# Optimization experiments

Hardware: AMD Instinct MI355X
Metric: run time of the kernel (lower is better)

The kernel has to match this reference:

```python
import jax, jax.numpy as jnp
import numpy as np

NUM_HEADS = 32
NUM_GROUP_HEADS = 8
DIM_MODEL = 2048
DIM_K = 64
DIM_V = 64


def setup_inputs() -> dict:
    key = jax.random.key(0)
    ks = jax.random.split(key, 11)
    B, S = 1, 2048
    scale = 0.02
    inp = {
        "queries": jax.random.normal(ks[0], (B, S, DIM_MODEL), jnp.float32),
        "keys": jax.random.normal(ks[1], (B, S, DIM_MODEL), jnp.float32),
        "values": jax.random.normal(ks[2], (B, S, DIM_MODEL), jnp.float32),
        "Wq": jax.random.normal(ks[3], (DIM_MODEL, DIM_K * NUM_HEADS), jnp.float32) * scale,
        "bq": jnp.zeros((DIM_K * NUM_HEADS,), jnp.float32),
        "Wk": jax.random.normal(ks[4], (DIM_MODEL, DIM_K * NUM_GROUP_HEADS), jnp.float32) * scale,
        "bk": jnp.zeros((DIM_K * NUM_GROUP_HEADS,), jnp.float32),
        "Wv": jax.random.normal(ks[5], (DIM_MODEL, DIM_V * NUM_GROUP_HEADS), jnp.float32) * scale,
        "bv": jnp.zeros((DIM_V * NUM_GROUP_HEADS,), jnp.float32),
        "Wo": jax.random.normal(ks[6], (DIM_V * NUM_HEADS, DIM_MODEL), jnp.float32) * scale,
        "bo": jnp.zeros((DIM_MODEL,), jnp.float32),
    }
    return inp


def reference(queries, keys, values, Wq, bq, Wk, bk, Wv, bv, Wo, bo):
    B, Sq, _ = queries.shape
    _, Sk, _ = keys.shape
    H, G = NUM_HEADS, NUM_GROUP_HEADS
    repeats = H // G

    # projections -> [B, heads, S, d]
    q = (queries @ Wq + bq).reshape(B, Sq, H, DIM_K).transpose(0, 2, 1, 3)
    k = (keys @ Wk + bk).reshape(B, Sk, G, DIM_K).transpose(0, 2, 1, 3)
    v = (values @ Wv + bv).reshape(B, Sk, G, DIM_V).transpose(0, 2, 1, 3)

    # GQA: repeat each group head `repeats` times (repeat_interleave on head dim)
    k = jnp.repeat(k, repeats, axis=1)  # [B, H, Sk, dk]
    v = jnp.repeat(v, repeats, axis=1)  # [B, H, Sk, dv]

    scores = jnp.einsum("bhqd,bhkd->bhqk", q, k) / (DIM_K ** 0.5)
    causal = jnp.triu(jnp.ones((Sq, Sk), dtype=bool), k=1)
    scores = jnp.where(causal, -jnp.inf, scores)
    attn = jax.nn.softmax(scores, axis=-1)
    out = jnp.einsum("bhqk,bhkd->bhqd", attn, v)  # [B, H, Sq, dv]
    out = out.transpose(0, 2, 1, 3).reshape(B, Sq, H * DIM_V)
    return out @ Wo + bo
```

## Files before the change

### kernel.cpp

```cpp
#include <hip/hip_runtime.h>
#include <hip/hip_bf16.h>

#define S_LEN  2048
#define DMODEL 2048
#define NH     32
#define NG     8
#define DK     64
#define DV     64

typedef short bf16x8 __attribute__((ext_vector_type(8)));
typedef float f32x4  __attribute__((ext_vector_type(4)));

__device__ __forceinline__ ushort f32_to_bf16(float f) {
    uint u = __float_as_uint(f);
    return (ushort)((u + 0x7fffu + ((u >> 16) & 1u)) >> 16);
}
__device__ __forceinline__ float bf16_to_f32(ushort h) {
    return __uint_as_float(((uint)h) << 16);
}
__device__ __forceinline__ uint pack_bf16x2(float a, float b) {
    return (uint)f32_to_bf16(a) | ((uint)f32_to_bf16(b) << 16);
}

__global__ void cast_f32_to_bf16(const float* __restrict__ in,
                                 ushort* __restrict__ out, int n8) {
    int i = blockIdx.x * blockDim.x + threadIdx.x;
    const int stride = gridDim.x * blockDim.x;
    for (; i < n8; i += stride) {
        const float4 a = ((const float4*)in)[2 * i];
        const float4 b = ((const float4*)in)[2 * i + 1];
        uint4 o;
        o.x = (uint)f32_to_bf16(a.x) | ((uint)f32_to_bf16(a.y) << 16);
        o.y = (uint)f32_to_bf16(a.z) | ((uint)f32_to_bf16(a.w) << 16);
        o.z = (uint)f32_to_bf16(b.x) | ((uint)f32_to_bf16(b.y) << 16);
        o.w = (uint)f32_to_bf16(b.z) | ((uint)f32_to_bf16(b.w) << 16);
        ((uint4*)out)[i] = o;
    }
}

__global__ void transpose_cast_bf16(const float* __restrict__ W,
                                    ushort* __restrict__ Wt, int K, int N) {
    __shared__ float t[32][33];
    const int n0 = blockIdx.x * 32, k0 = blockIdx.y * 32;
    const int tx = threadIdx.x, ty = threadIdx.y;
#pragma unroll
    for (int i = 0; i < 4; ++i)
        t[ty + 8 * i][tx] = W[(size_t)(k0 + ty + 8 * i) * N + n0 + tx];
    __syncthreads();
#pragma unroll
    for (int i = 0; i < 4; ++i)
        Wt[(size_t)(n0 + ty + 8 * i) * K + k0 + tx] = f32_to_bf16(t[tx][ty + 8 * i]);
}

__global__ void transpose_bf16(const ushort* __restrict__ in,
                               ushort* __restrict__ out, int R, int C) {
    __shared__ ushort t[32][34];
    const int c0 = blockIdx.x * 32, r0 = blockIdx.y * 32;
    const int tx = threadIdx.x, ty = threadIdx.y;
#pragma unroll
    for (int i = 0; i < 4; ++i)
        t[ty + 8 * i][tx] = in[(size_t)(r0 + ty + 8 * i) * C + c0 + tx];
    __syncthreads();
#pragma unroll
    for (int i = 0; i < 4; ++i)
        out[(size_t)(c0 + ty + 8 * i) * R + r0 + tx] = t[tx][ty + 8 * i];
}

template <bool OUT_F32>
__device__ __forceinline__ void gemm_body_128x64(
        const ushort* __restrict__ A, const ushort* __restrict__ Bt,
        const float* __restrict__ bias, void* __restrict__ Cv,
        ushort* As, ushort* Bs, int N, int K, float scale) {
    const int tid  = threadIdx.x;
    const int lane = tid & 63, wave = tid >> 6;
    const int l15 = lane & 15, quad = lane >> 4;
    const int row0 = blockIdx.y * 128, col0 = blockIdx.x * 64;

    f32x4 acc[2][4];
#pragma unroll
    for (int i = 0; i < 2; ++i)
#pragma unroll
        for (int j = 0; j < 4; ++j) { f32x4 z = {0.f,0.f,0.f,0.f}; acc[i][j] = z; }

    const int ar = tid >> 1, ak = (tid & 1) * 16;
    const int br = tid >> 2, bk = (tid & 3) * 8;
    const ushort* aptr = A  + (size_t)(row0 + ar) * K + ak;
    const ushort* bptr = Bt + (size_t)(col0 + br) * K + bk;

    bf16x8 a0 = *(const bf16x8*)(aptr);
    bf16x8 a1 = *(const bf16x8*)(aptr + 8);
    bf16x8 b0 = *(const bf16x8*)(bptr);

    for (int k0 = 0; k0 < K; k0 += 32) {
        __syncthreads();
        *(bf16x8*)&As[ar * 40 + ak]     = a0;
        *(bf16x8*)&As[ar * 40 + ak + 8] = a1;
        *(bf16x8*)&Bs[br * 40 + bk]     = b0;
        __syncthreads();

        if (k0 + 32 < K) {
            a0 = *(const bf16x8*)(aptr + k0 + 32);
            a1 = *(const bf16x8*)(aptr + k0 + 40);
            b0 = *(const bf16x8*)(bptr + k0 + 32);
        }

        bf16x8 af[2], bf[4];
#pragma unroll
        for (int mi = 0; mi < 2; ++mi)
            af[mi] = *(const bf16x8*)&As[(wave * 32 + mi * 16 + l15) * 40 + quad * 8];
#pragma unroll
        for (int ni = 0; ni < 4; ++ni)
            bf[ni] = *(const bf16x8*)&Bs[(ni * 16 + l15) * 40 + quad * 8];
#pragma unroll
        for (int mi = 0; mi < 2; ++mi)
#pragma unroll
            for (int ni = 0; ni < 4; ++ni)
                acc[mi][ni] = __builtin_amdgcn_mfma_f32_16x16x32_bf16(
                    af[mi], bf[ni], acc[mi][ni], 0, 0, 0);
    }

#pragma unroll
    for (int mi = 0; mi < 2; ++mi)
#pragma unroll
        for (int ni = 0; ni < 4; ++ni) {
            const int col = col0 + ni * 16 + l15;
            const float bv = bias[col];
#pragma unroll
            for (int reg = 0; reg < 4; ++reg) {
                const int row = row0 + wave * 32 + mi * 16 + quad * 4 + reg;
                const float val = (acc[mi][ni][reg] + bv) * scale;
                if (OUT_F32)
                    ((float*)Cv)[(size_t)row * N + col] = val;
                else
                    ((ushort*)Cv)[(size_t)row * N + col] = f32_to_bf16(val);
            }
        }
}

template <bool OUT_F32>
__global__ __launch_bounds__(256) void gemm_bf16_v2(
        const ushort* __restrict__ A, const ushort* __restrict__ Bt,
        const float* __restrict__ bias, void* __restrict__ Cv, int N, int K,
        float scale) {
    __shared__ ushort As[128 * 40];
    __shared__ ushort Bs[64 * 40];
    gemm_body_128x64<OUT_F32>(A, Bt, bias, Cv, As, Bs, N, K, scale);
}

__global__ __launch_bounds__(256) void gemm_kv(
        const ushort* __restrict__ Xk, const ushort* __restrict__ Xv,
        const ushort* __restrict__ Wkt, const ushort* __restrict__ Wvt,
        const float* __restrict__ bk, const float* __restrict__ bv,
        ushort* __restrict__ Kb, ushort* __restrict__ Vb, int N, int K) {
    __shared__ ushort As[128 * 40];
    __shared__ ushort Bs[64 * 40];
    if (blockIdx.z == 0)
        gemm_body_128x64<false>(Xk, Wkt, bk, Kb, As, Bs, N, K, 1.0f);
    else
        gemm_body_128x64<false>(Xv, Wvt, bv, Vb, As, Bs, N, K, 1.0f);
}

__global__ __launch_bounds__(256) void gqa_attn_mfma(
        const ushort* __restrict__ Qb, const ushort* __restrict__ Kb,
        const ushort* __restrict__ Vt, ushort* __restrict__ Ab) {
    __shared__ ushort Ks[64 * 72];
    __shared__ ushort Vs[64 * 72];
    __shared__ ushort Ps[4][16 * 72];

    const int h    = blockIdx.y, g = h >> 2;
    const int tid  = threadIdx.x;
    const int lane = tid & 63, wave = tid >> 6;
    const int l15  = lane & 15, quad = lane >> 4;
    const int NT   = S_LEN / 64;
    const float DEFER_THR = 11.5416f;

    const int srow = tid >> 2, sch = tid & 3;
    const ushort* kbase = Kb + (size_t)srow * (NG * DK) + g * DK + sch * 16;
    const ushort* vbase = Vt + (size_t)(g * 64 + srow) * S_LEN + sch * 16;

    for (int sel = 0; sel < 2; ++sel) {
        const int qt = sel ? (NT - 1 - (int)blockIdx.x) : (int)blockIdx.x;
        const int qr = qt * 64 + wave * 16;

        bf16x8 qa0, qa1;
        {
            const size_t base = (size_t)(qr + l15) * (NH * DK) + (size_t)h * DK + quad * 8;
            qa0 = *(const bf16x8*)&Qb[base];
            qa1 = *(const bf16x8*)&Qb[base + 32];
        }

        f32x4 o[4];
#pragma unroll
        for (int dt = 0; dt < 4; ++dt) { f32x4 z = {0.f,0.f,0.f,0.f}; o[dt] = z; }
        float m = -1e30f;
        float l = 0.f;

        bf16x8 kr0 = *(const bf16x8*)(kbase);
        bf16x8 kr1 = *(const bf16x8*)(kbase + 8);
        bf16x8 vr0 = *(const bf16x8*)(vbase);
        bf16x8 vr1 = *(const bf16x8*)(vbase + 8);

        for (int jt = 0; jt <= qt; ++jt) {
            __syncthreads();
            *(bf16x8*)&Ks[srow * 72 + sch * 16]     = kr0;
            *(bf16x8*)&Ks[srow * 72 + sch * 16 + 8] = kr1;
            *(bf16x8*)&Vs[srow * 72 + sch * 16]     = vr0;
            *(bf16x8*)&Vs[srow * 72 + sch * 16 + 8] = vr1;
            __syncthreads();

            if (jt < qt) {
                const size_t ko = (size_t)(jt + 1) * 64 * (NG * DK);
                const size_t vo = (size_t)(jt + 1) * 64;
                kr0 = *(const bf16x8*)(kbase + ko);
                kr1 = *(const bf16x8*)(kbase + ko + 8);
                vr0 = *(const bf16x8*)(vbase + vo);
                vr1 = *(const bf16x8*)(vbase + vo + 8);
            }

            f32x4 s[4];
#pragma unroll
            for (int kt = 0; kt < 4; ++kt) {
                const bf16x8 kb0 = *(const bf16x8*)&Ks[(kt * 16 + l15) * 72 + quad * 8];
                const bf16x8 kb1 = *(const bf16x8*)&Ks[(kt * 16 + l15) * 72 + 32 + quad * 8];
                f32x4 acc = {0.f, 0.f, 0.f, 0.f};
                acc = __builtin_amdgcn_mfma_f32_16x16x32_bf16(kb0, qa0, acc, 0, 0, 0);
                acc = __builtin_amdgcn_mfma_f32_16x16x32_bf16(kb1, qa1, acc, 0, 0, 0);
                s[kt] = acc;
            }

            if (jt == qt) {
                const int row = wave * 16 + l15;
#pragma unroll
                for (int kt = 0; kt < 4; ++kt)
#pragma unroll
                    for (int r = 0; r < 4; ++r) {
                        const int key = kt * 16 + quad * 4 + r;
                        if (key > row) s[kt][r] = -1e30f;
                    }
            }

            float pmax;
            {
                const float t0 = fmaxf(fmaxf(s[0][0], s[0][1]), fmaxf(s[0][2], s[0][3]));
                const float t1 = fmaxf(fmaxf(s[1][0], s[1][1]), fmaxf(s[1][2], s[1][3]));
                const float t2 = fmaxf(fmaxf(s[2][0], s[2][1]), fmaxf(s[2][2], s[2][3]));
                const float t3 = fmaxf(fmaxf(s[3][0], s[3][1]), fmaxf(s[3][2], s[3][3]));
                pmax = fmaxf(fmaxf(t0, t1), fmaxf(t2, t3));
            }
            pmax = fmaxf(pmax, __shfl_xor(pmax, 16, 64));
            pmax = fmaxf(pmax, __shfl_xor(pmax, 32, 64));

            if (!__all(pmax - m <= DEFER_THR)) {
                const float mnew  = fmaxf(m, pmax);
                const float alpha = __builtin_amdgcn_exp2f(m - mnew);
                l *= alpha;
#pragma unroll
                for (int dt = 0; dt < 4; ++dt)
#pragma unroll
                    for (int r = 0; r < 4; ++r) o[dt][r] *= alpha;
                m = mnew;
            }

            float p[4][4];
#pragma unroll
            for (int kt = 0; kt < 4; ++kt)
#pragma unroll
                for (int r = 0; r < 4; ++r)
                    p[kt][r] = __builtin_amdgcn_exp2f(s[kt][r] - m);

            float rsum;
            {
                const float u0 = (p[0][0] + p[0][1]) + (p[0][2] + p[0][3]);
                const float u1 = (p[1][0] + p[1][1]) + (p[1][2] + p[1][3]);
                const float u2 = (p[2][0] + p[2][1]) + (p[2][2] + p[2][3]);
                const float u3 = (p[3][0] + p[3][1]) + (p[3][2] + p[3][3]);
                rsum = (u0 + u1) + (u2 + u3);
            }
            rsum += __shfl_xor(rsum, 16, 64);
            rsum += __shfl_xor(rsum, 32, 64);
            l += rsum;

            ushort* Pw = &Ps[wave][0];
#pragma unroll
            for (int kt = 0; kt < 4; ++kt) {
                uint2 uu;
                uu.x = pack_bf16x2(p[kt][0], p[kt][1]);
                uu.y = pack_bf16x2(p[kt][2], p[kt][3]);
                *(uint2*)&Pw[l15 * 72 + kt * 16 + quad * 4] = uu;
            }
            const bf16x8 pa0 = *(const bf16x8*)&Pw[l15 * 72 + quad * 8];
            const bf16x8 pa1 = *(const bf16x8*)&Pw[l15 * 72 + 32 + quad * 8];

#pragma unroll
            for (int dt = 0; dt < 4; ++dt) {
                const bf16x8 vb0 = *(const bf16x8*)&Vs[(dt * 16 + l15) * 72 + quad * 8];
                const bf16x8 vb1 = *(const bf16x8*)&Vs[(dt * 16 + l15) * 72 + 32 + quad * 8];
                o[dt] = __builtin_amdgcn_mfma_f32_16x16x32_bf16(vb0, pa0, o[dt], 0, 0, 0);
                o[dt] = __builtin_amdgcn_mfma_f32_16x16x32_bf16(vb1, pa1, o[dt], 0, 0, 0);
            }
        }

        const float invl = 1.0f / l;
#pragma unroll
        for (int dt = 0; dt < 4; ++dt) {
            uint2 uu;
            uu.x = pack_bf16x2(o[dt][0] * invl, o[dt][1] * invl);
            uu.y = pack_bf16x2(o[dt][2] * invl, o[dt][3] * invl);
            *(uint2*)&Ab[(size_t)(qr + l15) * (NH * DV) + (size_t)h * DV + dt * 16 + quad * 4] = uu;
        }
    }
}

extern "C" void kernel_launch(void* const* d_in, const int* in_sizes, int n_in,
                              void* d_out, int out_size, void* d_ws, size_t ws_size,
                              hipStream_t stream) {
    const float* queries = (const float*)d_in[0];
    const float* keys    = (const float*)d_in[1];
    const float* values  = (const float*)d_in[2];
    const float* Wq      = (const float*)d_in[3];
    const float* bq      = (const float*)d_in[4];
    const float* Wk      = (const float*)d_in[5];
    const float* bk      = (const float*)d_in[6];
    const float* Wv      = (const float*)d_in[7];
    const float* bv      = (const float*)d_in[8];
    const float* Wo      = (const float*)d_in[9];
    const float* bo      = (const float*)d_in[10];
    float* out = (float*)d_out;

    const size_t MB = 1024 * 1024;
    unsigned char* w = (unsigned char*)d_ws;
    ushort* Xq  = (ushort*)(w + 0 * MB);
    ushort* Xk  = (ushort*)(w + 8 * MB);
    ushort* Xv  = (ushort*)(w + 16 * MB);
    ushort* Wqt = (ushort*)(w + 24 * MB);
    ushort* Wkt = (ushort*)(w + 32 * MB);
    ushort* Wvt = (ushort*)(w + 34 * MB);
    ushort* Wot = (ushort*)(w + 36 * MB);
    ushort* Qb  = (ushort*)(w + 44 * MB);
    ushort* Kb  = (ushort*)(w + 52 * MB);
    ushort* Vb  = (ushort*)(w + 54 * MB);
    ushort* Ab  = (ushort*)(w + 56 * MB);
    ushort* Vtp = (ushort*)(w + 8 * MB);

    const int n8 = (S_LEN * DMODEL) / 8;
    cast_f32_to_bf16<<<1024, 256, 0, stream>>>(queries, Xq, n8);
    cast_f32_to_bf16<<<1024, 256, 0, stream>>>(keys,    Xk, n8);
    cast_f32_to_bf16<<<1024, 256, 0, stream>>>(values,  Xv, n8);

    dim3 tb(32, 8);
    transpose_cast_bf16<<<dim3(2048 / 32, 2048 / 32), tb, 0, stream>>>(Wq, Wqt, DMODEL, 2048);
    transpose_cast_bf16<<<dim3(512 / 32,  2048 / 32), tb, 0, stream>>>(Wk, Wkt, DMODEL, 512);
    transpose_cast_bf16<<<dim3(512 / 32,  2048 / 32), tb, 0, stream>>>(Wv, Wvt, DMODEL, 512);
    transpose_cast_bf16<<<dim3(2048 / 32, 2048 / 32), tb, 0, stream>>>(Wo, Wot, DMODEL, 2048);

    const float QSCALE = 0.125f * 1.44269504f;
    gemm_bf16_v2<false><<<dim3(2048 / 64, 2048 / 128), 256, 0, stream>>>(
        Xq, Wqt, bq, Qb, 2048, DMODEL, QSCALE);
    gemm_kv<<<dim3(512 / 64, 2048 / 128, 2), 256, 0, stream>>>(
        Xk, Xv, Wkt, Wvt, bk, bv, Kb, Vb, 512, DMODEL);

    transpose_bf16<<<dim3(512 / 32, 2048 / 32), tb, 0, stream>>>(Vb, Vtp, S_LEN, 512);

    gqa_attn_mfma<<<dim3(16, 32), 256, 0, stream>>>(Qb, Kb, Vtp, Ab);

    gemm_bf16_v2<true><<<dim3(2048 / 64, 2048 / 128), 256, 0, stream>>>(
        Ab, Wot, bo, out, 2048, DMODEL, 1.0f);
}
```

Baseline: 303.3 us.

## Use direct global-to-LDS loads with double-buffered tiles in bf16 GEMMs

The projection GEMM body now loads A and B tiles with global_load_lds straight into shared memory instead of going through registers. It double-buffers the tiles so the next k-slice is fetched while MFMAs run on the current one, which removes one __syncthreads per iteration and the register staging. The trade-off is that the LDS layout loses its padding (row stride 32 instead of 40), so fragment reads may now hit bank conflicts. Correctness also depends on the barrier waiting for the outstanding async LDS loads.

```diff
diff --git a/kernel.cpp b/kernel.cpp
--- a/kernel.cpp
+++ b/kernel.cpp
@@ -20,6 +20,12 @@
 }
 __device__ __forceinline__ uint pack_bf16x2(float a, float b) {
     return (uint)f32_to_bf16(a) | ((uint)f32_to_bf16(b) << 16);
+}
+
+typedef __attribute__((address_space(3))) uint lds_uint;
+typedef const __attribute__((address_space(1))) uint g_uint;
+__device__ __forceinline__ void gload16(const void* g, void* l) {
+    __builtin_amdgcn_global_load_lds((g_uint*)g, (lds_uint*)l, 16, 0, 0);
 }
 
 __global__ void cast_f32_to_bf16(const float* __restrict__ in,
@@ -70,7 +76,8 @@
 __device__ __forceinline__ void gemm_body_128x64(
         const ushort* __restrict__ A, const ushort* __restrict__ Bt,
         const float* __restrict__ bias, void* __restrict__ Cv,
-        ushort* As, ushort* Bs, int N, int K, float scale) {
+        ushort* As, ushort* Bs,
+        int N, int K, float scale) {
     const int tid  = threadIdx.x;
     const int lane = tid & 63, wave = tid >> 6;
     const int l15 = lane & 15, quad = lane >> 4;
@@ -82,41 +89,45 @@
 #pragma unroll
         for (int j = 0; j < 4; ++j) { f32x4 z = {0.f,0.f,0.f,0.f}; acc[i][j] = z; }
 
-    const int ar = tid >> 1, ak = (tid & 1) * 16;
-    const int br = tid >> 2, bk = (tid & 3) * 8;
-    const ushort* aptr = A  + (size_t)(row0 + ar) * K + ak;
-    const ushort* bptr = Bt + (size_t)(col0 + br) * K + bk;
-
-    bf16x8 a0 = *(const bf16x8*)(aptr);
-    bf16x8 a1 = *(const bf16x8*)(aptr + 8);
-    bf16x8 b0 = *(const bf16x8*)(bptr);
-
+    const int sr = wave * 16 + (lane >> 2);
+    const int sc = (lane & 3) * 8;
+    const ushort* ga0 = A  + (size_t)(row0 + sr) * K + sc;
+    const ushort* ga1 = A  + (size_t)(row0 + 64 + sr) * K + sc;
+    const ushort* gb0 = Bt + (size_t)(col0 + sr) * K + sc;
+    ushort* lA0 = As + wave * 512;
+    ushort* lA1 = As + 2048 + wave * 512;
+    ushort* lB0 = Bs + wave * 512;
+
+    gload16(ga0, lA0);
+    gload16(ga1, lA1);
+    gload16(gb0, lB0);
+
+    int cur = 0;
     for (int k0 = 0; k0 < K; k0 += 32) {
         __syncthreads();
-        *(bf16x8*)&As[ar * 40 + ak]     = a0;
-        *(bf16x8*)&As[ar * 40 + ak + 8] = a1;
-        *(bf16x8*)&Bs[br * 40 + bk]     = b0;
-        __syncthreads();
-
         if (k0 + 32 < K) {
-            a0 = *(const bf16x8*)(aptr + k0 + 32);
-            a1 = *(const bf16x8*)(aptr + k0 + 40);
-            b0 = *(const bf16x8*)(bptr + k0 + 32);
-        }
+            const int nxt = cur ^ 1;
+            gload16(ga0 + k0 + 32, lA0 + nxt * 4096);
+            gload16(ga1 + k0 + 32, lA1 + nxt * 4096);
+            gload16(gb0 + k0 + 32, lB0 + nxt * 2048);
+        }
+        const ushort* Ac = As + cur * 4096;
+        const ushort* Bc = Bs + cur * 2048;
 
         bf16x8 af[2], bf[4];
 #pragma unroll
         for (int mi = 0; mi < 2; ++mi)
-            af[mi] = *(const bf16x8*)&As[(wave * 32 + mi * 16 + l15) * 40 + quad * 8];
+            af[mi] = *(const bf16x8*)&Ac[(wave * 32 + mi * 16 + l15) * 32 + quad * 8];
 #pragma unroll
         for (int ni = 0; ni < 4; ++ni)
-            bf[ni] = *(const bf16x8*)&Bs[(ni * 16 + l15) * 40 + quad * 8];
+            bf[ni] = *(const bf16x8*)&Bc[(ni * 16 + l15) * 32 + quad * 8];
 #pragma unroll
         for (int mi = 0; mi < 2; ++mi)
 #pragma unroll
             for (int ni = 0; ni < 4; ++ni)
                 acc[mi][ni] = __builtin_amdgcn_mfma_f32_16x16x32_bf16(
                     af[mi], bf[ni], acc[mi][ni], 0, 0, 0);
+        cur ^= 1;
     }
 
 #pragma unroll
@@ -142,8 +153,8 @@
         const ushort* __restrict__ A, const ushort* __restrict__ Bt,
         const float* __restrict__ bias, void* __restrict__ Cv, int N, int K,
         float scale) {
-    __shared__ ushort As[128 * 40];
-    __shared__ ushort Bs[64 * 40];
+    __shared__ ushort As[2 * 128 * 32];
+    __shared__ ushort Bs[2 * 64 * 32];
     gemm_body_128x64<OUT_F32>(A, Bt, bias, Cv, As, Bs, N, K, scale);
 }
 
@@ -152,8 +163,8 @@
         const ushort* __restrict__ Wkt, const ushort* __restrict__ Wvt,
         const float* __restrict__ bk, const float* __restrict__ bv,
         ushort* __restrict__ Kb, ushort* __restrict__ Vb, int N, int K) {
-    __shared__ ushort As[128 * 40];
-    __shared__ ushort Bs[64 * 40];
+    __shared__ ushort As[2 * 128 * 32];
+    __shared__ ushort Bs[2 * 64 * 32];
     if (blockIdx.z == 0)
         gemm_body_128x64<false>(Xk, Wkt, bk, Kb, As, Bs, N, K, 1.0f);
     else
```

Result: slower. 309.9 us (+2.2%).

## Merge cast, weight-transpose and QKV GEMM launches; fuse V transpose into epilogue

Applied to the files above, without the earlier changes.

The three input casts become one launch over a z-grid, and the four weight transpose-casts become one launch. The Q, K and V projections run as a single GEMM launch. The V projection writes its output already transposed through a shared-memory staging tile, so the separate V transpose kernel goes away. This cuts kernel launch count and one global round trip of V. The cost is idle blocks in the merged QKV grid (z=1,2 only use 8 of 32 x-blocks) and a larger shared-memory footprint.

```diff
diff --git a/kernel.cpp b/kernel.cpp
--- a/kernel.cpp
+++ b/kernel.cpp
@@ -22,8 +22,14 @@
     return (uint)f32_to_bf16(a) | ((uint)f32_to_bf16(b) << 16);
 }
 
-__global__ void cast_f32_to_bf16(const float* __restrict__ in,
-                                 ushort* __restrict__ out, int n8) {
+__global__ void cast3_f32_to_bf16(const float* __restrict__ q,
+                                  const float* __restrict__ k,
+                                  const float* __restrict__ v,
+                                  ushort* __restrict__ xq,
+                                  ushort* __restrict__ xk,
+                                  ushort* __restrict__ xv, int n8) {
+    const float* in  = blockIdx.z == 0 ? q  : (blockIdx.z == 1 ? k  : v);
+    ushort*      out = blockIdx.z == 0 ? xq : (blockIdx.z == 1 ? xk : xv);
     int i = blockIdx.x * blockDim.x + threadIdx.x;
     const int stride = gridDim.x * blockDim.x;
     for (; i < n8; i += stride) {
@@ -38,10 +44,20 @@
     }
 }
 
-__global__ void transpose_cast_bf16(const float* __restrict__ W,
-                                    ushort* __restrict__ Wt, int K, int N) {
+__global__ void transpose_cast4(const float* __restrict__ Wq,
+                                const float* __restrict__ Wk,
+                                const float* __restrict__ Wv,
+                                const float* __restrict__ Wo,
+                                ushort* __restrict__ Wqt, ushort* __restrict__ Wkt,
+                                ushort* __restrict__ Wvt, ushort* __restrict__ Wot) {
     __shared__ float t[32][33];
-    const int n0 = blockIdx.x * 32, k0 = blockIdx.y * 32;
+    int bx = blockIdx.x;
+    const float* W; ushort* Wt; int N;
+    if (bx < 64)      { W = Wq; Wt = Wqt; N = 2048; }
+    else if (bx < 80) { W = Wk; Wt = Wkt; N = 512;  bx -= 64; }
+    else if (bx < 96) { W = Wv; Wt = Wvt; N = 512;  bx -= 80; }
+    else              { W = Wo; Wt = Wot; N = 2048; bx -= 96; }
+    const int n0 = bx * 32, k0 = blockIdx.y * 32;
     const int tx = threadIdx.x, ty = threadIdx.y;
 #pragma unroll
     for (int i = 0; i < 4; ++i)
@@ -49,28 +65,14 @@
     __syncthreads();
 #pragma unroll
     for (int i = 0; i < 4; ++i)
-        Wt[(size_t)(n0 + ty + 8 * i) * K + k0 + tx] = f32_to_bf16(t[tx][ty + 8 * i]);
-}
-
-__global__ void transpose_bf16(const ushort* __restrict__ in,
-                               ushort* __restrict__ out, int R, int C) {
-    __shared__ ushort t[32][34];
-    const int c0 = blockIdx.x * 32, r0 = blockIdx.y * 32;
-    const int tx = threadIdx.x, ty = threadIdx.y;
-#pragma unroll
-    for (int i = 0; i < 4; ++i)
-        t[ty + 8 * i][tx] = in[(size_t)(r0 + ty + 8 * i) * C + c0 + tx];
-    __syncthreads();
-#pragma unroll
-    for (int i = 0; i < 4; ++i)
-        out[(size_t)(c0 + ty + 8 * i) * R + r0 + tx] = t[tx][ty + 8 * i];
-}
-
-template <bool OUT_F32>
+        Wt[(size_t)(n0 + ty + 8 * i) * 2048 + k0 + tx] = f32_to_bf16(t[tx][ty + 8 * i]);
+}
+
+template <int MODE>
 __device__ __forceinline__ void gemm_body_128x64(
         const ushort* __restrict__ A, const ushort* __restrict__ Bt,
         const float* __restrict__ bias, void* __restrict__ Cv,
-        ushort* As, ushort* Bs, int N, int K, float scale) {
+        ushort* As, ushort* Bs, ushort* Ts, int N, int K, float scale) {
     const int tid  = threadIdx.x;
     const int lane = tid & 63, wave = tid >> 6;
     const int l15 = lane & 15, quad = lane >> 4;
@@ -119,6 +121,31 @@
                     af[mi], bf[ni], acc[mi][ni], 0, 0, 0);
     }
 
+    if (MODE == 2) {
+        __syncthreads();
+#pragma unroll
+        for (int mi = 0; mi < 2; ++mi)
+#pragma unroll
+            for (int ni = 0; ni < 4; ++ni) {
+                const float bv = bias[col0 + ni * 16 + l15];
+                const int lrow = wave * 32 + mi * 16 + quad * 4;
+                uint2 uu;
+                uu.x = pack_bf16x2((acc[mi][ni][0] + bv) * scale,
+                                   (acc[mi][ni][1] + bv) * scale);
+                uu.y = pack_bf16x2((acc[mi][ni][2] + bv) * scale,
+                                   (acc[mi][ni][3] + bv) * scale);
+                *(uint2*)&Ts[(ni * 16 + l15) * 136 + lrow] = uu;
+            }
+        __syncthreads();
+        const int v = tid >> 2, s0 = (tid & 3) * 32;
+#pragma unroll
+        for (int i = 0; i < 4; ++i) {
+            const uint4 d = *(const uint4*)&Ts[v * 136 + s0 + 8 * i];
+            *(uint4*)&((ushort*)Cv)[(size_t)(col0 + v) * S_LEN + row0 + s0 + 8 * i] = d;
+        }
+        return;
+    }
+
 #pragma unroll
     for (int mi = 0; mi < 2; ++mi)
 #pragma unroll
@@ -129,7 +156,7 @@
             for (int reg = 0; reg < 4; ++reg) {
                 const int row = row0 + wave * 32 + mi * 16 + quad * 4 + reg;
                 const float val = (acc[mi][ni][reg] + bv) * scale;
-                if (OUT_F32)
+                if (MODE == 1)
                     ((float*)Cv)[(size_t)row * N + col] = val;
                 else
                     ((ushort*)Cv)[(size_t)row * N + col] = f32_to_bf16(val);
@@ -137,27 +164,34 @@
         }
 }
 
-template <bool OUT_F32>
-__global__ __launch_bounds__(256) void gemm_bf16_v2(
+__global__ __launch_bounds__(256) void gemm_o(
         const ushort* __restrict__ A, const ushort* __restrict__ Bt,
-        const float* __restrict__ bias, void* __restrict__ Cv, int N, int K,
-        float scale) {
-    __shared__ ushort As[128 * 40];
-    __shared__ ushort Bs[64 * 40];
-    gemm_body_128x64<OUT_F32>(A, Bt, bias, Cv, As, Bs, N, K, scale);
-}
-
-__global__ __launch_bounds__(256) void gemm_kv(
-        const ushort* __restrict__ Xk, const ushort* __restrict__ Xv,
-        const ushort* __restrict__ Wkt, const ushort* __restrict__ Wvt,
-        const float* __restrict__ bk, const float* __restrict__ bv,
-        ushort* __restrict__ Kb, ushort* __restrict__ Vb, int N, int K) {
-    __shared__ ushort As[128 * 40];
-    __shared__ ushort Bs[64 * 40];
-    if (blockIdx.z == 0)
-        gemm_body_128x64<false>(Xk, Wkt, bk, Kb, As, Bs, N, K, 1.0f);
-    else
-        gemm_body_128x64<false>(Xv, Wvt, bv, Vb, As, Bs, N, K, 1.0f);
+        const float* __restrict__ bias, float* __restrict__ Cv, int N, int K) {
+    __shared__ ushort smem[128 * 40 + 64 * 40];
+    gemm_body_128x64<1>(A, Bt, bias, Cv, smem, smem + 128 * 40, nullptr, N, K, 1.0f);
+}
+
+__global__ __launch_bounds__(256) void gemm_qkv(
+        const ushort* __restrict__ Xq, const ushort* __restrict__ Xk,
+        const ushort* __restrict__ Xv,
+        const ushort* __restrict__ Wqt, const ushort* __restrict__ Wkt,
+        const ushort* __restrict__ Wvt,
+        const float* __restrict__ bq, const float* __restrict__ bk,
+        const float* __restrict__ bv,
+        ushort* __restrict__ Qb, ushort* __restrict__ Kb,
+        ushort* __restrict__ Vtp, int K, float qscale) {
+    __shared__ ushort smem[64 * 136];
+    ushort* As = smem;
+    ushort* Bs = smem + 128 * 40;
+    const int z = blockIdx.z;
+    if (z == 0) {
+        gemm_body_128x64<0>(Xq, Wqt, bq, Qb, As, Bs, nullptr, 2048, K, qscale);
+    } else if (blockIdx.x < 8) {
+        if (z == 1)
+            gemm_body_128x64<0>(Xk, Wkt, bk, Kb, As, Bs, nullptr, 512, K, 1.0f);
+        else
+            gemm_body_128x64<2>(Xv, Wvt, bv, Vtp, As, Bs, smem, 512, K, 1.0f);
+    }
 }
 
 __global__ __launch_bounds__(256) void gqa_attn_mfma(
@@ -338,31 +372,23 @@
     ushort* Wot = (ushort*)(w + 36 * MB);
     ushort* Qb  = (ushort*)(w + 44 * MB);
     ushort* Kb  = (ushort*)(w + 52 * MB);
-    ushort* Vb  = (ushort*)(w + 54 * MB);
+    ushort* Vtp = (ushort*)(w + 54 * MB);
     ushort* Ab  = (ushort*)(w + 56 * MB);
-    ushort* Vtp = (ushort*)(w + 8 * MB);
 
     const int n8 = (S_LEN * DMODEL) / 8;
-    cast_f32_to_bf16<<<1024, 256, 0, stream>>>(queries, Xq, n8);
-    cast_f32_to_bf16<<<1024, 256, 0, stream>>>(keys,    Xk, n8);
-    cast_f32_to_bf16<<<1024, 256, 0, stream>>>(values,  Xv, n8);
+    cast3_f32_to_bf16<<<dim3(1024, 1, 3), 256, 0, stream>>>(
+        queries, keys, values, Xq, Xk, Xv, n8);
 
     dim3 tb(32, 8);
-    transpose_cast_bf16<<<dim3(2048 / 32, 2048 / 32), tb, 0, stream>>>(Wq, Wqt, DMODEL, 2048);
-    transpose_cast_bf16<<<dim3(512 / 32,  2048 / 32), tb, 0, stream>>>(Wk, Wkt, DMODEL, 512);
-    transpose_cast_bf16<<<dim3(512 / 32,  2048 / 32), tb, 0, stream>>>(Wv, Wvt, DMODEL, 512);
-    transpose_cast_bf16<<<dim3(2048 / 32, 2048 / 32), tb, 0, stream>>>(Wo, Wot, DMODEL, 2048);
+    transpose_cast4<<<dim3(160, 64), tb, 0, stream>>>(
+        Wq, Wk, Wv, Wo, Wqt, Wkt, Wvt, Wot);
 
     const float QSCALE = 0.125f * 1.44269504f;
-    gemm_bf16_v2<false><<<dim3(2048 / 64, 2048 / 128), 256, 0, stream>>>(
-        Xq, Wqt, bq, Qb, 2048, DMODEL, QSCALE);
-    gemm_kv<<<dim3(512 / 64, 2048 / 128, 2), 256, 0, stream>>>(
-        Xk, Xv, Wkt, Wvt, bk, bv, Kb, Vb, 512, DMODEL);
-
-    transpose_bf16<<<dim3(512 / 32, 2048 / 32), tb, 0, stream>>>(Vb, Vtp, S_LEN, 512);
+    gemm_qkv<<<dim3(32, 16, 3), 256, 0, stream>>>(
+        Xq, Xk, Xv, Wqt, Wkt, Wvt, bq, bk, bv, Qb, Kb, Vtp, DMODEL, QSCALE);
 
     gqa_attn_mfma<<<dim3(16, 32), 256, 0, stream>>>(Qb, Kb, Vtp, Ab);
 
-    gemm_bf16_v2<true><<<dim3(2048 / 64, 2048 / 128), 256, 0, stream>>>(
-        Ab, Wot, bo, out, 2048, DMODEL, 1.0f);
-}
+    gemm_o<<<dim3(2048 / 64, 2048 / 128), 256, 0, stream>>>(
+        Ab, Wot, bo, out, 2048, DMODEL);
+}
```

Result: slower. 319.7 us (+5.4%).
